# Optimization experiments

Measured on AMD Instinct MI355X. Metric: run time of the kernel, lower is better.

The kernel has to match this reference:

```python
import jax, jax.numpy as jnp
import numpy as np

N_OBJS = 100          # max detections / scatter buffer size
TOP_K = 100           # top_k_n peaks per channel
KP_THRES = 0.3        # score threshold before NMS
NMS_IOU = 0.5
RESIZE_H, RESIZE_W = 1536.0, 1536.0   # resize_shape (== heatmap HxW here)
H, W = 1536, 1536


def _peak_hms(hms):
    # 3x3 stride-1 SAME max pool; keep only local maxima (Base.apply_max_pool)
    hmax = jax.lax.reduce_window(hms, -jnp.inf, jax.lax.max, (1, 3, 3, 1), (1, 1, 1, 1), 'SAME')
    return jnp.where(hms == hmax, hms, 0.0)


def _top_k_loc(hms, k):
    # per-channel top-k peak coordinates -> [b, c, k, 2] (y, x) int32
    b, h, w, c = hms.shape
    flat = jnp.transpose(hms, (0, 3, 1, 2)).reshape(b, c, h * w)
    _, idx = jax.lax.top_k(flat, k)
    return jnp.stack([idx // w, idx % w], axis=-1).astype(jnp.int32)


def _iou_matrix(boxes):
    # boxes [N,4] = (y1,x1,y2,x2)
    y1, x1, y2, x2 = boxes[:, 0], boxes[:, 1], boxes[:, 2], boxes[:, 3]
    area = jnp.maximum(y2 - y1, 0.0) * jnp.maximum(x2 - x1, 0.0)
    iy1 = jnp.maximum(y1[:, None], y1[None, :]); ix1 = jnp.maximum(x1[:, None], x1[None, :])
    iy2 = jnp.minimum(y2[:, None], y2[None, :]); ix2 = jnp.minimum(x2[:, None], x2[None, :])
    inter = jnp.maximum(iy2 - iy1, 0.0) * jnp.maximum(ix2 - ix1, 0.0)
    union = area[:, None] + area[None, :] - inter
    return inter / jnp.maximum(union, 1e-8)


def _nms_single(boxes, scores):
    # greedy single-class NMS, fixed-size (combined_non_max_suppression equivalent,
    # clip_boxes=False, score_threshold=-inf); padded slots are zeros like TF.
    order = jnp.argsort(-scores)
    boxes, scores = boxes[order], scores[order]
    n = boxes.shape[0]
    iou = _iou_matrix(boxes)
    idxs = jnp.arange(n)

    def step(suppressed, inp):
        i, iou_row = inp
        keep_i = ~suppressed[i]
        return suppressed | (keep_i & (iou_row > NMS_IOU) & (idxs > i)), keep_i

    _, keep = jax.lax.scan(step, jnp.zeros(n, bool), (idxs, iou))
    perm = jnp.argsort(jnp.where(keep, 0, 1))  # stable: compact kept to front, score order preserved
    keep_s = keep[perm]
    out_boxes = jnp.where(keep_s[:, None], boxes[perm], 0.0)
    out_scores = jnp.where(keep_s, scores[perm], 0.0)
    return out_boxes, out_scores, jnp.zeros(n, jnp.float32)


def _forward(obj_heat_map, offset_map, size_maps, origin_shapes):
    resize_shape = jnp.array([RESIZE_H, RESIZE_W], jnp.float32)
    ratio = origin_shapes / resize_shape                      # [b,2]
    hms = _peak_hms(obj_heat_map)                             # [b,H,W,2]
    b = hms.shape[0]
    coors = _top_k_loc(hms, TOP_K)                            # [b,2,K,2]
    b_coors, b_lnmks = coors[:, :1], coors[:, 1:]             # obj / nose coords
    bidx = jnp.arange(b)[:, None, None]

    # nose landmark: scores at nose-channel peaks, masked mean of coords (int mean like TF)
    nose_scores = hms[bidx, b_lnmks[..., 0], b_lnmks[..., 1], 1]     # [b,1,K]
    nose_mask = nose_scores > 0.5
    cnt = jnp.maximum(jnp.sum(nose_mask), 1)
    lnmk_mean = jnp.sum(jnp.where(nose_mask[..., None], b_lnmks, 0), axis=(0, 1, 2)) // cnt
    b_lnmks_m = lnmk_mean.reshape(b, 1, 2)                    # requires b == 1 (as in original)
    b_nose_scores = jnp.where(nose_mask, nose_scores, -1.0).reshape(b, -1)

    # boxes from sizes at object peaks
    size_vals = size_maps[bidx, b_coors[..., 0], b_coors[..., 1]]    # [b,1,K,2]
    obj_scores = hms[bidx, b_coors[..., 0], b_coors[..., 1], 0]      # [b,1,K]
    centers = b_coors.astype(jnp.float32)
    tls = jnp.maximum(centers - size_vals / 2.0, 0.0)
    brs = jnp.minimum(centers + size_vals / 2.0, resize_shape - 1.0)
    bboxes = jnp.concatenate([tls, brs], axis=-1) * jnp.tile(ratio, (1, 2))[:, None, None, :]
    bboxes, scores = bboxes[:, 0], obj_scores[:, 0]           # [b,K,4], [b,K]

    # scatter masked candidates into -1-initialized buffer (tensor_scatter_nd_update equivalent)
    mask = scores > KP_THRES
    cand = jnp.where(mask[..., None], jnp.concatenate([bboxes, scores[..., None]], -1), -1.0)
    cand = jnp.pad(cand, ((0, 0), (0, N_OBJS - TOP_K), (0, 0)), constant_values=-1.0)  # [b,N_OBJS,5]

    nb, ns, nc = jax.vmap(_nms_single)(cand[..., :4], cand[..., 4])
    box_results = jnp.where(nb == -1.0, jnp.inf, nb)
    box_results = jnp.where(box_results == 0.0, jnp.inf, box_results)  # (x - 1 == -1)
    b_bboxes = jnp.concatenate([box_results, ns[..., None], nc[..., None]], axis=-1)  # [b,N_OBJS,6]

    # offset vectors at the mean nose landmark (gather 8ch -> [b,n,4,2])
    bidx2 = jnp.arange(b)[:, None]
    off = offset_map[bidx2, b_lnmks_m[..., 0], b_lnmks_m[..., 1]].reshape(b, 1, 4, 2)
    lf = b_lnmks_m.astype(jnp.float32)
    b_ENM = (lf[:, :, None, :] - off) * ratio[:, None, None, :]
    b_lnmks_out = lf * ratio[:, None, :]
    return b_bboxes, b_lnmks_out, b_ENM, b_nose_scores


def setup_inputs() -> dict:
    key = jax.random.key(0)
    k1, k2, k3 = jax.random.split(key, 3)
    obj_heat_map = jax.random.uniform(k1, (1, H, W, 2), jnp.float32)
    offset_map = jax.random.normal(k2, (1, H, W, 8), jnp.float32) * 8.0
    size_maps = jax.random.uniform(k3, (1, H, W, 2), jnp.float32) * 128.0
    origin_shapes = jnp.array([[1080.0, 1920.0]], jnp.float32)
    return {"obj_heat_map": obj_heat_map, "offset_map": offset_map,
            "size_maps": size_maps, "origin_shapes": origin_shapes}


def reference(obj_heat_map, offset_map, size_maps, origin_shapes):
    return _forward(obj_heat_map, offset_map, size_maps, origin_shapes)
```

## Files before the change

### kernel.cpp

```cpp
#include <hip/hip_runtime.h>
#include <cstdint>

#define IW 1536
#define IH 1536
#define TOPK 100
#define CAPP 327680
#define CAPB 128
#define CAPT 8192
#define BF_INF16 0x7F7Fu

#define NBLK 192
#define VBTOT 576

typedef unsigned u32; typedef unsigned long long u64; typedef unsigned short u16;

#define OH1   0
#define OCNT  4096
#define OSEL  4102
#define OLSD  4106
#define OBAR  4170
#define OZEND 4172
#define OPK   4172
#define OPV   (OPK + 2*CAPP)
#define OLB   (OPV + CAPP)
#define OLT   (OLB + 4*CAPB)

__device__ __forceinline__ u32 enc16(u32 b){ b &= 0xFFFFu; return (b & 0x8000u) ? ((~b)&0xFFFFu) : (b|0x8000u); }
__device__ __forceinline__ u32 dec16(u32 e){ return (e & 0x8000u) ? (e^0x8000u) : ((~e)&0xFFFFu); }
__device__ __forceinline__ float up16(u32 b){ return __uint_as_float((b&0xFFFFu)<<16); }
__device__ __forceinline__ u16 f2bf(float f){ u32 u=__float_as_uint(f); return (u16)((u + 0x7FFFu + ((u>>16)&1u))>>16); }

__device__ __forceinline__ void wave_sel2048(const u32* bins, u32 need, int* Dout, u32* Aout){
  int lane = threadIdx.x & 63;
  u32 s = 0;
  #pragma unroll
  for(int k=0;k<32;++k) s += bins[lane*32+k];
  u32 c = s;
  #pragma unroll
  for(int off=1;off<64;off<<=1){
    u32 v = __shfl_down(c, off, 64);
    if(lane + off < 64) c += v;
  }
  u32 cnext = __shfl_down(c, 1, 64); if(lane==63) cnext = 0u;
  u64 m = __ballot(c >= need);
  if(m == 0ull){ if(lane==0){ *Dout = 0; *Aout = 0u; } return; }
  int L = 63 - __builtin_clzll((unsigned long long)m);
  if(lane == L){
    u32 above = cnext; int D = 32*L;
    for(int b=32*L+31; b>=32*L; --b){
      u32 h = bins[b];
      if(above + h >= need){ D = b; break; }
      above += h;
    }
    *Dout = D; *Aout = above;
  }
}

union SMem {
  struct {
    u32 lh[4096];
    u32 lbuf[2][1600];
    u16 vbuf[2][1600];
  } a;
  struct {
    u32 lhh[4096];
    u64 tbuf[2][2048];
    u32 lsdl[64];
  } b;
  struct {
    u32 tidxS[2][CAPT];
    u32 h2s[2][2048];
    u64 keysS[2][CAPB];
    u32 selS[2][CAPB];
    u32 wbitsS[2][64];
    u32 lsdS[64];
    u32 hdr[10];
    float oval[TOPK]; int oidx[TOPK];
    float nval[TOPK]; int nidx[TOPK];
    float cbox[TOPK][4]; float cscore[TOPK]; float area[TOPK];
    int sup[TOPK]; int slotv[TOPK];
    u64 nbits[2*TOPK];
  } c;
};

__global__ __launch_bounds__(1024, 4) void fused_kernel(
    const u32* __restrict__ hm, u32* __restrict__ ws,
    const u32* __restrict__ szm, const u16* __restrict__ offm,
    const u16* __restrict__ orig, u16* __restrict__ out){
  __shared__ SMem S;
  __shared__ u32 lcnt[2], lbase[2], tcnt[2], tbase[2];
  __shared__ int Dsh[2]; __shared__ u32 Ash[2];
  __shared__ int selcS[2], selc2S[2], BvS[2], LshS[2], tcS[2];
  __shared__ u64 suppS[2];
  __shared__ int cS, srS, scS, meanr, meanc;

  int tid = threadIdx.x, lane = tid & 63;

  for(int i=tid;i<4096;i+=1024) S.a.lh[i]=0u;
  for(int vb = blockIdx.x; vb < VBTOT; vb += NBLK){
    __syncthreads();
    if(tid<2) lcnt[tid]=0u;
    __syncthreads();

    int p = (vb*1024 + tid)*4;
    int y = p / IW, x = p - y*IW;
    const u32* R1 = hm + y*IW;
    const u32* R0 = y ? R1 - IW : R1;
    const u32* R2 = (y < IH-1) ? R1 + IW : R1;
    uint4 c0 = *(const uint4*)(R0+x), c1 = *(const uint4*)(R1+x), c2 = *(const uint4*)(R2+x);
    int xl = x ? x-1 : 0, xr = (x+4 < IW) ? x+4 : IW-1;
    u32 a0[6] = {R0[xl], c0.x, c0.y, c0.z, c0.w, R0[xr]};
    u32 a1[6] = {R1[xl], c1.x, c1.y, c1.z, c1.w, R1[xr]};
    u32 a2[6] = {R2[xl], c2.x, c2.y, c2.z, c2.w, R2[xr]};

    #pragma unroll
    for(int j=0;j<4;++j){
      u32 cc = a1[j+1];
      u32 cl = cc & 0xFFFFu, chv = cc >> 16;
      u32 m0=0u, m1=0u;
      #pragma unroll
      for(int d=0;d<3;++d){
        u32 n0=a0[j+d], n2=a2[j+d]; u32 t;
        t=n0&0xFFFFu; m0=t>m0?t:m0;  t=n0>>16; m1=t>m1?t:m1;
        t=n2&0xFFFFu; m0=t>m0?t:m0;  t=n2>>16; m1=t>m1?t:m1;
      }
      { u32 n=a1[j];   u32 t=n&0xFFFFu; m0=t>m0?t:m0; t=n>>16; m1=t>m1?t:m1; }
      { u32 n=a1[j+2]; u32 t=n&0xFFFFu; m0=t>m0?t:m0; t=n>>16; m1=t>m1?t:m1; }
      bool pk0 = (cl >= m0), pk1 = (chv >= m1);
      u32 idx = (u32)(p + j);

      u64 mk0 = __ballot(pk0);
      if(mk0){
        u32 cw = __popcll(mk0), b;
        if(lane==0) b = atomicAdd(&lcnt[0], cw);
        b = __shfl(b, 0);
        if(pk0){
          u32 pos = b + __popcll(mk0 & ((1ull<<lane)-1ull));
          if(pos < 1600){ S.a.lbuf[0][pos] = idx; S.a.vbuf[0][pos] = (u16)cl; }
        }
      }
      u64 mk1 = __ballot(pk1);
      if(mk1){
        u32 cw = __popcll(mk1), b;
        if(lane==0) b = atomicAdd(&lcnt[1], cw);
        b = __shfl(b, 0);
        if(pk1){
          u32 pos = b + __popcll(mk1 & ((1ull<<lane)-1ull));
          if(pos < 1600){ S.a.lbuf[1][pos] = idx; S.a.vbuf[1][pos] = (u16)chv; }
        }
      }
      if(pk0) atomicAdd(&S.a.lh[enc16(cl)>>5], 1u);
      if(pk1) atomicAdd(&S.a.lh[2048 + (enc16(chv)>>5)], 1u);
    }
    __syncthreads();
    if(tid < 2){
      u32 n = lcnt[tid]; if(n > 1600) n = 1600;
      lcnt[tid] = n;
      lbase[tid] = atomicAdd(&ws[OCNT+tid], n);
    }
    __syncthreads();
    {
      u16* pvw = (u16*)(ws + OPV);
      for(int ch2=0;ch2<2;++ch2){
        u32 n = lcnt[ch2], base = lbase[ch2];
        for(u32 i=tid;i<n;i+=1024){
          u32 g = base + i;
          if(g < CAPP){ ws[OPK + ch2*CAPP + g] = S.a.lbuf[ch2][i]; pvw[ch2*CAPP + g] = S.a.vbuf[ch2][i]; }
        }
      }
    }
  }
  __syncthreads();
  for(int i=tid;i<4096;i+=1024) if(S.a.lh[i]) atomicAdd(&ws[OH1+i], S.a.lh[i]);

  __syncthreads();
  if(tid==0){
    __hip_atomic_fetch_add(&ws[OBAR], 1u, __ATOMIC_RELEASE, __HIP_MEMORY_SCOPE_AGENT);
    while(__hip_atomic_load(&ws[OBAR], __ATOMIC_ACQUIRE, __HIP_MEMORY_SCOPE_AGENT) < (u32)NBLK)
      __builtin_amdgcn_s_sleep(2);
  }
  __syncthreads();

  for(int i=tid;i<4096;i+=1024) S.b.lhh[i] = ws[OH1+i];
  if(tid < 2) tcnt[tid] = 0u;
  if(tid < 64) S.b.lsdl[tid] = 0u;
  __syncthreads();
  if(tid < 64)       wave_sel2048(S.b.lhh,        (u32)TOPK, &Dsh[0], &Ash[0]);
  else if(tid < 128) wave_sel2048(S.b.lhh + 2048, (u32)TOPK, &Dsh[1], &Ash[1]);
  __syncthreads();
  if(blockIdx.x == 0 && tid < 2){ ws[OSEL+tid] = (u32)Dsh[tid]; ws[OSEL+2+tid] = Ash[tid]; }

  {
    const u16* pvr = (const u16*)(ws + OPV);
    u64* listBw = (u64*)(ws + OLB);
    for(int ch2=0;ch2<2;++ch2){
      u32 n = ws[OCNT+ch2]; if(n > CAPP) n = CAPP;
      int D2 = Dsh[ch2];
      for(u32 base = blockIdx.x*1024; base < n; base += (u32)NBLK*1024){
        u32 i = base + tid;
        bool act = (i < n);
        u32 e = 0, idx = 0;
        if(act){ e = enc16(pvr[ch2*CAPP + i]); idx = ws[OPK + ch2*CAPP + i]; }
        if(act && (int)(e>>5) > D2){
          u32 pos = atomicAdd(&ws[OCNT+2+ch2], 1u);
          if(pos < CAPB) listBw[ch2*CAPB + pos] = ((u64)e<<32) | (u32)(~idx);
        }
        bool isT = act && ((int)(e>>5) == D2);
        if(isT) atomicAdd(&S.b.lsdl[ch2*32 + (e & 31u)], 1u);
        u64 mk = __ballot(isT);
        if(mk){
          u32 cw = __popcll(mk), b;
          if(lane==0) b = atomicAdd(&tcnt[ch2], cw);
          b = __shfl(b, 0);
          if(isT){
            u32 pos = b + __popcll(mk & ((1ull<<lane)-1ull));
            if(pos < 2048) S.b.tbuf[ch2][pos] = ((u64)e<<32) | (u32)(~idx);
          }
        }
      }
    }
  }
  __syncthreads();
  if(tid < 2){
    u32 c = tcnt[tid]; if(c > 2048) c = 2048;
    tcnt[tid] = c;
    tbase[tid] = atomicAdd(&ws[OCNT+4+tid], c);
  }
  __syncthreads();
  {
    u64* tieW = (u64*)(ws + OLT);
    for(int ch2=0;ch2<2;++ch2)
      for(u32 i=tid;i<tcnt[ch2];i+=1024){
        u32 g = tbase[ch2] + i;
        if(g < CAPT) tieW[ch2*CAPT + g] = S.b.tbuf[ch2][i];
      }
  }
  if(tid < 64 && S.b.lsdl[tid]) atomicAdd(&ws[OLSD + tid], S.b.lsdl[tid]);

  __syncthreads();
  if(blockIdx.x != 0){
    if(tid==0) __hip_atomic_fetch_add(&ws[OBAR+1], 1u, __ATOMIC_RELEASE, __HIP_MEMORY_SCOPE_AGENT);
    return;
  }
  if(tid==0){
    __hip_atomic_fetch_add(&ws[OBAR+1], 1u, __ATOMIC_RELEASE, __HIP_MEMORY_SCOPE_AGENT);
    while(__hip_atomic_load(&ws[OBAR+1], __ATOMIC_ACQUIRE, __HIP_MEMORY_SCOPE_AGENT) < (u32)NBLK)
      __builtin_amdgcn_s_sleep(2);
  }
  __syncthreads();

  {
    bool act5 = (tid < 512);
    int ch = (tid >> 8) & 1, ltid = tid & 255;

    if(tid < 10) S.c.hdr[tid] = ws[OCNT + tid];
    if(tid < 64) S.c.lsdS[tid] = ws[OLSD + tid];
    for(int i=tid;i<4096;i+=1024) ((u32*)S.c.h2s)[i] = 0u;
    if(tid < 128) ((u32*)S.c.wbitsS)[tid] = 0u;
    if(tid < 4){ selcS[tid&1] = 0; selc2S[tid&1] = 0; }
    if(tid < 2){ BvS[tid] = 0; LshS[tid] = 0; tcS[tid] = 0; }
    if(tid < TOPK){ S.c.oval[tid]=0.0f; S.c.oidx[tid]=0; S.c.nval[tid]=0.0f; S.c.nidx[tid]=0; }
    __syncthreads();

    int nB=0, nT=0, D=0; u32 above=0;
    const u64* listB = nullptr; const u64* tie = nullptr;
    float* dval = nullptr; int* didx = nullptr;
    if(act5){
      nB = (int)S.c.hdr[2+ch]; if(nB > CAPB) nB = CAPB;
      nT = (int)S.c.hdr[4+ch]; if(nT > CAPT) nT = CAPT;
      D  = (int)S.c.hdr[6+ch];
      above = S.c.hdr[8+ch];
      listB = ((const u64*)(ws + OLB)) + ch*CAPB;
      tie   = ((const u64*)(ws + OLT)) + ch*CAPT;
      dval = ch ? S.c.nval : S.c.oval;
      didx = ch ? S.c.nidx : S.c.oidx;
    }

    if(act5 && ltid < 64){
      u32 h = (lane < 32) ? S.c.lsdS[ch*32 + lane] : 0u;
      u32 c = h;
      #pragma unroll
      for(int off=1;off<32;off<<=1){
        u32 v = __shfl_down(c, off, 64);
        if(lane + off < 32) c += v;
      }
      u32 need2 = (u32)TOPK - above;
      u64 m = __ballot(lane >= 1 && lane < 32 && c >= need2);
      if(lane == 0){
        LshS[ch] = m ? (63 - __builtin_clzll((unsigned long long)m)) : 0;
        selcS[ch] = nB;
      }
    }
    if(act5) for(int i=ltid;i<nB;i+=256) S.c.keysS[ch][i] = listB[i];
    __syncthreads();
    u32 thr = 0; float tval = 0.0f;
    if(act5){ thr = ((u32)D<<5) | (u32)LshS[ch]; tval = up16(dec16(thr)); }

    if(act5) for(int base2=0; base2<nT; base2+=256){
      int i = base2 + ltid;
      bool act = (i < nT);
      u64 k = 0; u32 e = 0, idx = 0;
      if(act){ k = tie[i]; e = (u32)(k>>32); idx = ~(u32)(k & 0xFFFFFFFFu); }
      if(act && e > thr){
        int pos = atomicAdd(&selcS[ch], 1); if(pos < CAPB) S.c.keysS[ch][pos] = k;
      }
      bool isT = act && (e == thr);
      u64 mk = __ballot(isT);
      if(mk){
        u32 cw = __popcll(mk), b;
        if(lane==0) b = (u32)atomicAdd(&tcS[ch], (int)cw);
        b = __shfl(b, 0);
        if(isT){
          u32 pos = b + __popcll(mk & ((1ull<<lane)-1ull));
          if(pos < CAPT) S.c.tidxS[ch][pos] = idx;
        }
      }
      if(isT) atomicAdd(&S.c.h2s[ch][idx>>11], 1u);
    }
    __syncthreads();

    int nA = 0, need = 0;
    if(act5){
      nA = selcS[ch]; if(nA > CAPB) nA = CAPB; if(nA > TOPK) nA = TOPK;
      need = TOPK - nA;
      if(ltid < nA){
        u64 kreg = S.c.keysS[ch][ltid];
        int r = 0;
        for(int j=0;j<nA;++j) r += (S.c.keysS[ch][j] > kreg);
        if(r < TOPK){
          dval[r] = up16(dec16((u32)(kreg>>32)));
          didx[r] = (int)(~(u32)(kreg & 0xFFFFFFFFu));
        }
      }
      if(ltid < 64){
        const u32* hh = S.c.h2s[ch];
        int base = lane*32;
        u32 s = 0;
        #pragma unroll
        for(int k2=0;k2<32;++k2) s += hh[base+k2];
        u32 c = s;
        #pragma unroll
        for(int off=1;off<64;off<<=1){
          u32 v = __shfl_up(c, off, 64);
          if(lane >= off) c += v;
        }
        u64 m = __ballot(need > 0 && c >= (u32)need);
        int L = m ? (int)(__ffsll((unsigned long long)m) - 1) : -1;
        if(L >= 0 && lane == L){
          u32 hb[32];
          #pragma unroll
          for(int k2=0;k2<32;++k2) hb[k2] = hh[base+k2];
          u32 cum2 = c - s;
          int Bsel = base;
          #pragma unroll
          for(int k2=0;k2<32;++k2){
            if(cum2 + hb[k2] >= (u32)need){ Bsel = base+k2; break; }
            cum2 += hb[k2];
          }
          BvS[ch] = Bsel;
        }
      }
    }
    __syncthreads();

    int B = 0, tc = 0;
    if(act5){
      B = BvS[ch];
      tc = tcS[ch]; if(tc > CAPT) tc = CAPT;
      if(need > 0){
        for(int i=ltid;i<tc;i+=256){
          u32 idx = S.c.tidxS[ch][i];
          int b = (int)(idx>>11);
          if(b < B){
            int pos = atomicAdd(&selc2S[ch], 1);
            if(pos < CAPB) S.c.selS[ch][pos] = idx;
          } else if(b == B){
            atomicOr(&S.c.wbitsS[ch][(idx&2047)>>5], 1u<<(idx&31));
          }
        }
      }
    }
    __syncthreads();

    if(act5){
      int sc = selc2S[ch]; if(sc > CAPB) sc = CAPB;
      if(need > 0 && ltid < sc){
        u32 v = S.c.selS[ch][ltid];
        int r = 0;
        for(int j=0;j<sc;++j) r += (S.c.selS[ch][j] < v);
        if(nA + r < TOPK){ dval[nA+r] = tval; didx[nA+r] = (int)v; }
      }
      if(need > 0 && ltid < 64){
        u32 bits = S.c.wbitsS[ch][ltid];
        u32 cnt = __popc(bits);
        u32 incl = cnt;
        #pragma unroll
        for(int off=1;off<64;off<<=1){
          u32 v = __shfl_up(incl, off, 64);
          if(lane >= off) incl += v;
        }
        int excl = (int)(incl - cnt);
        int rem = need - sc;
        int pos = nA + sc + excl;
        int j = 0;
        while(bits){
          int l = __ffs(bits) - 1; bits &= bits - 1;
          if(excl + j < rem && pos + j < TOPK){
            dval[pos+j] = tval;
            didx[pos+j] = (int)(((u32)B<<11) | ((u32)ltid<<5) | (u32)l);
          }
          ++j;
        }
      }
    }
    __syncthreads();

    float ry = up16(orig[0]) / 1536.0f;
    float rx = up16(orig[1]) / 1536.0f;

    if(tid == 0){ cS = 0; srS = 0; scS = 0; }
    __syncthreads();
    if(tid < TOPK && S.c.nval[tid] > 0.5f){
      atomicAdd(&cS, 1);
      atomicAdd(&srS, S.c.nidx[tid] / IW);
      atomicAdd(&scS, S.c.nidx[tid] % IW);
    }
    if(tid < TOPK) out[610 + tid] = f2bf(S.c.nval[tid] > 0.5f ? S.c.nval[tid] : -1.0f);
    __syncthreads();
    if(tid == 0){
      int c = cS < 1 ? 1 : cS;
      meanr = srS / c; meanc = scS / c;
    }

    if(tid < TOPK){
      int idx = S.c.oidx[tid];
      int r = idx / IW, c = idx - r*IW;
      float score = S.c.oval[tid];
      u32 sz = szm[idx];
      float sy = up16(sz), sx = up16(sz>>16);
      float cy = (float)r, cx = (float)c;
      float tly = fmaxf(cy - sy*0.5f, 0.0f);
      float tlx = fmaxf(cx - sx*0.5f, 0.0f);
      float bry = fminf(cy + sy*0.5f, 1535.0f);
      float brx = fminf(cx + sx*0.5f, 1535.0f);
      bool mk = score > 0.3f;
      float b0 = mk ? tly*ry : -1.0f;
      float b1 = mk ? tlx*rx : -1.0f;
      float b2 = mk ? bry*ry : -1.0f;
      float b3 = mk ? brx*rx : -1.0f;
      S.c.cbox[tid][0]=b0; S.c.cbox[tid][1]=b1; S.c.cbox[tid][2]=b2; S.c.cbox[tid][3]=b3;
      S.c.cscore[tid] = mk ? score : -1.0f;
      S.c.area[tid] = fmaxf(b2-b0,0.0f) * fmaxf(b3-b1,0.0f);
    }
    if(tid < 2*TOPK) S.c.nbits[tid] = 0ull;
    __syncthreads();

    for(int t=tid; t<TOPK*TOPK; t+=1024){
      int i = t / TOPK, j = t - i*TOPK;
      if(j > i){
        float iy1 = fmaxf(S.c.cbox[i][0], S.c.cbox[j][0]);
        float ix1 = fmaxf(S.c.cbox[i][1], S.c.cbox[j][1]);
        float iy2 = fminf(S.c.cbox[i][2], S.c.cbox[j][2]);
        float ix2 = fminf(S.c.cbox[i][3], S.c.cbox[j][3]);
        float inter = fmaxf(iy2-iy1,0.0f) * fmaxf(ix2-ix1,0.0f);
        float uni = (S.c.area[i] + S.c.area[j]) - inter;
        if(inter / fmaxf(uni, 1e-8f) > 0.5f)
          atomicOr(&S.c.nbits[i*2 + (j>>6)], 1ull << (j&63));
      }
    }
    __syncthreads();
    if(tid == 0){
      u64 s0 = 0ull, s1 = 0ull;
      for(int base=0;base<TOPK;base+=10){
        u64 buf[20];
        #pragma unroll
        for(int k=0;k<20;++k) buf[k] = S.c.nbits[2*base+k];
        #pragma unroll
        for(int k=0;k<10;++k){
          int i = base+k;
          bool su = (i<64) ? ((s0>>i)&1ull) : ((s1>>(i-64))&1ull);
          if(!su){ s0 |= buf[2*k]; s1 |= buf[2*k+1]; }
        }
      }
      suppS[0] = s0; suppS[1] = s1;
    }
    __syncthreads();
    if(tid < TOPK) S.c.sup[tid] = (int)((suppS[tid>>6] >> (tid&63)) & 1ull);
    __syncthreads();

    if(tid < TOPK){
      int kbefore = 0, sbefore = 0, ktot = 0;
      for(int j=0;j<TOPK;++j){
        int sj = S.c.sup[j];
        ktot += (1 - sj);
        if(j < tid){ kbefore += (1 - sj); sbefore += sj; }
      }
      int slot = S.c.sup[tid] ? (ktot + sbefore) : kbefore;
      S.c.slotv[slot] = tid;
    }
    __syncthreads();

    if(tid < TOPK){
      int s = S.c.slotv[tid];
      bool ks = !S.c.sup[s];
      u16 row[6];
      if(ks){
        for(int d=0;d<4;++d){
          float v = S.c.cbox[s][d];
          row[d] = (v == -1.0f || v == 0.0f) ? (u16)BF_INF16 : f2bf(v);
        }
        row[4] = f2bf(S.c.cscore[s]);
      } else {
        for(int d=0;d<4;++d) row[d] = (u16)BF_INF16;
        row[4] = 0;
      }
      row[5] = 0;
      for(int d=0;d<6;++d) out[tid*6 + d] = row[d];
    }

    if(tid == 0){
      float lfy = (float)meanr, lfx = (float)meanc;
      out[600] = f2bf(lfy * ry);
      out[601] = f2bf(lfx * rx);
      const u16* op = offm + ((size_t)meanr*IW + meanc)*8;
      for(int p=0;p<4;++p){
        out[602 + p*2 + 0] = f2bf((lfy - up16(op[p*2+0])) * ry);
        out[602 + p*2 + 1] = f2bf((lfx - up16(op[p*2+1])) * rx);
      }
    }
  }
}

extern "C" void kernel_launch(void* const* d_in, const int* in_sizes, int n_in,
                              void* d_out, int out_size, void* d_ws, size_t ws_size,
                              hipStream_t stream) {
  const u32* heat = (const u32*)d_in[0];
  const u16* offm = (const u16*)d_in[1];
  const u32* szm  = (const u32*)d_in[2];
  const u16* orig = (const u16*)d_in[3];
  u16* out = (u16*)d_out;
  u32* ws = (u32*)d_ws;

  hipMemsetAsync(ws, 0, OZEND*sizeof(u32), stream);
  fused_kernel<<<NBLK, 1024, 0, stream>>>(heat, ws, szm, offm, orig, out);
}
```

Measured before the change: 197.3 us.

## Use dynamic work stealing, wider grid and per-channel final blocks

Raises the grid from 192 to 448 blocks. Heatmap chunks are now claimed through a global atomic counter, so blocks balance the peak-finding work themselves. The candidate scan becomes a single pass per block. The final top-k/NMS stage is split so block 0 handles the object channel and block 1 the nose channel, instead of one block running both. To make room, the large shared tie-index buffer moves to global workspace and the other shared buffers shrink, which should let more blocks stay resident. The grid-wide spin barriers now depend on all 448 blocks being co-resident, and the tighter launch bounds may force register spills.

```diff
diff --git a/kernel.cpp b/kernel.cpp
--- a/kernel.cpp
+++ b/kernel.cpp
@@ -9,7 +9,7 @@
 #define CAPT 8192
 #define BF_INF16 0x7F7Fu
 
-#define NBLK 192
+#define NBLK 448
 #define VBTOT 576
 
 typedef unsigned u32; typedef unsigned long long u64; typedef unsigned short u16;
@@ -19,8 +19,9 @@
 #define OSEL  4102
 #define OLSD  4106
 #define OBAR  4170
-#define OZEND 4172
-#define OPK   4172
+#define OWRK  4172
+#define OZEND 4176
+#define OPK   4176
 #define OPV   (OPK + 2*CAPP)
 #define OLB   (OPV + CAPP)
 #define OLT   (OLB + 4*CAPB)
@@ -64,43 +65,52 @@
   } a;
   struct {
     u32 lhh[4096];
-    u64 tbuf[2][2048];
+    u64 tbuf[2][1024];
     u32 lsdl[64];
   } b;
   struct {
-    u32 tidxS[2][CAPT];
-    u32 h2s[2][2048];
-    u64 keysS[2][CAPB];
-    u32 selS[2][CAPB];
-    u32 wbitsS[2][64];
-    u32 lsdS[64];
+    u32 h2s[2048];
+    u64 keysS[CAPB];
+    u32 selS[CAPB];
+    u32 wbitsS[64];
+    u32 lsdS[32];
     u32 hdr[10];
-    float oval[TOPK]; int oidx[TOPK];
-    float nval[TOPK]; int nidx[TOPK];
+    float val[TOPK]; int vidx[TOPK];
     float cbox[TOPK][4]; float cscore[TOPK]; float area[TOPK];
     int sup[TOPK]; int slotv[TOPK];
     u64 nbits[2*TOPK];
   } c;
 };
 
-__global__ __launch_bounds__(1024, 4) void fused_kernel(
+__device__ __forceinline__ void grid_arrive(u32* ctr){
+  __hip_atomic_fetch_add(ctr, 1u, __ATOMIC_RELEASE, __HIP_MEMORY_SCOPE_AGENT);
+}
+__device__ __forceinline__ void grid_wait(u32* ctr, u32 target){
+  while(__hip_atomic_load(ctr, __ATOMIC_ACQUIRE, __HIP_MEMORY_SCOPE_AGENT) < target)
+    __builtin_amdgcn_s_sleep(2);
+}
+
+__global__ __launch_bounds__(1024, 8) void fused_kernel(
     const u32* __restrict__ hm, u32* __restrict__ ws,
     const u32* __restrict__ szm, const u16* __restrict__ offm,
     const u16* __restrict__ orig, u16* __restrict__ out){
   __shared__ SMem S;
   __shared__ u32 lcnt[2], lbase[2], tcnt[2], tbase[2];
   __shared__ int Dsh[2]; __shared__ u32 Ash[2];
-  __shared__ int selcS[2], selc2S[2], BvS[2], LshS[2], tcS[2];
+  __shared__ int selcS, selc2S, BvS, LshS, tcS, vbS;
   __shared__ u64 suppS[2];
-  __shared__ int cS, srS, scS, meanr, meanc;
+  __shared__ int cS, srS, scS;
 
   int tid = threadIdx.x, lane = tid & 63;
 
   for(int i=tid;i<4096;i+=1024) S.a.lh[i]=0u;
-  for(int vb = blockIdx.x; vb < VBTOT; vb += NBLK){
-    __syncthreads();
+  for(;;){
+    __syncthreads();
+    if(tid==0) vbS = (int)atomicAdd(&ws[OWRK], 1u);
     if(tid<2) lcnt[tid]=0u;
     __syncthreads();
+    int vb = vbS;
+    if(vb >= VBTOT) break;
 
     int p = (vb*1024 + tid)*4;
     int y = p / IW, x = p - y*IW;
@@ -170,15 +180,10 @@
       }
     }
   }
-  __syncthreads();
   for(int i=tid;i<4096;i+=1024) if(S.a.lh[i]) atomicAdd(&ws[OH1+i], S.a.lh[i]);
 
   __syncthreads();
-  if(tid==0){
-    __hip_atomic_fetch_add(&ws[OBAR], 1u, __ATOMIC_RELEASE, __HIP_MEMORY_SCOPE_AGENT);
-    while(__hip_atomic_load(&ws[OBAR], __ATOMIC_ACQUIRE, __HIP_MEMORY_SCOPE_AGENT) < (u32)NBLK)
-      __builtin_amdgcn_s_sleep(2);
-  }
+  if(tid==0){ grid_arrive(&ws[OBAR]); grid_wait(&ws[OBAR], (u32)NBLK); }
   __syncthreads();
 
   for(int i=tid;i<4096;i+=1024) S.b.lhh[i] = ws[OH1+i];
@@ -196,33 +201,31 @@
     for(int ch2=0;ch2<2;++ch2){
       u32 n = ws[OCNT+ch2]; if(n > CAPP) n = CAPP;
       int D2 = Dsh[ch2];
-      for(u32 base = blockIdx.x*1024; base < n; base += (u32)NBLK*1024){
-        u32 i = base + tid;
-        bool act = (i < n);
-        u32 e = 0, idx = 0;
-        if(act){ e = enc16(pvr[ch2*CAPP + i]); idx = ws[OPK + ch2*CAPP + i]; }
-        if(act && (int)(e>>5) > D2){
-          u32 pos = atomicAdd(&ws[OCNT+2+ch2], 1u);
-          if(pos < CAPB) listBw[ch2*CAPB + pos] = ((u64)e<<32) | (u32)(~idx);
-        }
-        bool isT = act && ((int)(e>>5) == D2);
-        if(isT) atomicAdd(&S.b.lsdl[ch2*32 + (e & 31u)], 1u);
-        u64 mk = __ballot(isT);
-        if(mk){
-          u32 cw = __popcll(mk), b;
-          if(lane==0) b = atomicAdd(&tcnt[ch2], cw);
-          b = __shfl(b, 0);
-          if(isT){
-            u32 pos = b + __popcll(mk & ((1ull<<lane)-1ull));
-            if(pos < 2048) S.b.tbuf[ch2][pos] = ((u64)e<<32) | (u32)(~idx);
-          }
+      u32 i = blockIdx.x*1024 + tid;
+      bool act = (i < n);
+      u32 e = 0, idx = 0;
+      if(act){ e = enc16(pvr[ch2*CAPP + i]); idx = ws[OPK + ch2*CAPP + i]; }
+      if(act && (int)(e>>5) > D2){
+        u32 pos = atomicAdd(&ws[OCNT+2+ch2], 1u);
+        if(pos < CAPB) listBw[ch2*CAPB + pos] = ((u64)e<<32) | (u32)(~idx);
+      }
+      bool isT = act && ((int)(e>>5) == D2);
+      if(isT) atomicAdd(&S.b.lsdl[ch2*32 + (e & 31u)], 1u);
+      u64 mk = __ballot(isT);
+      if(mk){
+        u32 cw = __popcll(mk), b;
+        if(lane==0) b = atomicAdd(&tcnt[ch2], cw);
+        b = __shfl(b, 0);
+        if(isT){
+          u32 pos = b + __popcll(mk & ((1ull<<lane)-1ull));
+          if(pos < 1024) S.b.tbuf[ch2][pos] = ((u64)e<<32) | (u32)(~idx);
         }
       }
     }
   }
   __syncthreads();
   if(tid < 2){
-    u32 c = tcnt[tid]; if(c > 2048) c = 2048;
+    u32 c = tcnt[tid]; if(c > 1024) c = 1024;
     tcnt[tid] = c;
     tbase[tid] = atomicAdd(&ws[OCNT+4+tid], c);
   }
@@ -238,46 +241,32 @@
   if(tid < 64 && S.b.lsdl[tid]) atomicAdd(&ws[OLSD + tid], S.b.lsdl[tid]);
 
   __syncthreads();
-  if(blockIdx.x != 0){
-    if(tid==0) __hip_atomic_fetch_add(&ws[OBAR+1], 1u, __ATOMIC_RELEASE, __HIP_MEMORY_SCOPE_AGENT);
-    return;
-  }
-  if(tid==0){
-    __hip_atomic_fetch_add(&ws[OBAR+1], 1u, __ATOMIC_RELEASE, __HIP_MEMORY_SCOPE_AGENT);
-    while(__hip_atomic_load(&ws[OBAR+1], __ATOMIC_ACQUIRE, __HIP_MEMORY_SCOPE_AGENT) < (u32)NBLK)
-      __builtin_amdgcn_s_sleep(2);
-  }
+  if(tid==0) grid_arrive(&ws[OBAR+1]);
+  if(blockIdx.x >= 2) return;
+  if(tid==0) grid_wait(&ws[OBAR+1], (u32)NBLK);
   __syncthreads();
 
   {
-    bool act5 = (tid < 512);
-    int ch = (tid >> 8) & 1, ltid = tid & 255;
+    int ch = (int)blockIdx.x;
 
     if(tid < 10) S.c.hdr[tid] = ws[OCNT + tid];
-    if(tid < 64) S.c.lsdS[tid] = ws[OLSD + tid];
-    for(int i=tid;i<4096;i+=1024) ((u32*)S.c.h2s)[i] = 0u;
-    if(tid < 128) ((u32*)S.c.wbitsS)[tid] = 0u;
-    if(tid < 4){ selcS[tid&1] = 0; selc2S[tid&1] = 0; }
-    if(tid < 2){ BvS[tid] = 0; LshS[tid] = 0; tcS[tid] = 0; }
-    if(tid < TOPK){ S.c.oval[tid]=0.0f; S.c.oidx[tid]=0; S.c.nval[tid]=0.0f; S.c.nidx[tid]=0; }
-    __syncthreads();
-
-    int nB=0, nT=0, D=0; u32 above=0;
-    const u64* listB = nullptr; const u64* tie = nullptr;
-    float* dval = nullptr; int* didx = nullptr;
-    if(act5){
-      nB = (int)S.c.hdr[2+ch]; if(nB > CAPB) nB = CAPB;
-      nT = (int)S.c.hdr[4+ch]; if(nT > CAPT) nT = CAPT;
-      D  = (int)S.c.hdr[6+ch];
-      above = S.c.hdr[8+ch];
-      listB = ((const u64*)(ws + OLB)) + ch*CAPB;
-      tie   = ((const u64*)(ws + OLT)) + ch*CAPT;
-      dval = ch ? S.c.nval : S.c.oval;
-      didx = ch ? S.c.nidx : S.c.oidx;
-    }
-
-    if(act5 && ltid < 64){
-      u32 h = (lane < 32) ? S.c.lsdS[ch*32 + lane] : 0u;
+    if(tid < 32) S.c.lsdS[tid] = ws[OLSD + ch*32 + tid];
+    for(int i=tid;i<2048;i+=1024) S.c.h2s[i] = 0u;
+    if(tid < 64) S.c.wbitsS[tid] = 0u;
+    if(tid == 0){ selcS = 0; selc2S = 0; BvS = 0; LshS = 0; tcS = 0; }
+    if(tid < TOPK){ S.c.val[tid]=0.0f; S.c.vidx[tid]=0; }
+    __syncthreads();
+
+    int nB = (int)S.c.hdr[2+ch]; if(nB > CAPB) nB = CAPB;
+    int nT = (int)S.c.hdr[4+ch]; if(nT > CAPT) nT = CAPT;
+    int D  = (int)S.c.hdr[6+ch];
+    u32 above = S.c.hdr[8+ch];
+    const u64* listB = ((const u64*)(ws + OLB)) + ch*CAPB;
+    const u64* tie   = ((const u64*)(ws + OLT)) + ch*CAPT;
+    u32* tidxG = ws + OPK + ch*CAPT;
+
+    if(tid < 64){
+      u32 h = (lane < 32) ? S.c.lsdS[lane] : 0u;
       u32 c = h;
       #pragma unroll
       for(int off=1;off<32;off<<=1){
@@ -287,130 +276,122 @@
       u32 need2 = (u32)TOPK - above;
       u64 m = __ballot(lane >= 1 && lane < 32 && c >= need2);
       if(lane == 0){
-        LshS[ch] = m ? (63 - __builtin_clzll((unsigned long long)m)) : 0;
-        selcS[ch] = nB;
-      }
-    }
-    if(act5) for(int i=ltid;i<nB;i+=256) S.c.keysS[ch][i] = listB[i];
-    __syncthreads();
-    u32 thr = 0; float tval = 0.0f;
-    if(act5){ thr = ((u32)D<<5) | (u32)LshS[ch]; tval = up16(dec16(thr)); }
-
-    if(act5) for(int base2=0; base2<nT; base2+=256){
-      int i = base2 + ltid;
+        LshS = m ? (63 - __builtin_clzll((unsigned long long)m)) : 0;
+        selcS = nB;
+      }
+    }
+    for(int i=tid;i<nB;i+=1024) S.c.keysS[i] = listB[i];
+    __syncthreads();
+    u32 thr = ((u32)D<<5) | (u32)LshS;
+    float tval = up16(dec16(thr));
+
+    for(int base2=0; base2<nT; base2+=1024){
+      int i = base2 + tid;
       bool act = (i < nT);
       u64 k = 0; u32 e = 0, idx = 0;
       if(act){ k = tie[i]; e = (u32)(k>>32); idx = ~(u32)(k & 0xFFFFFFFFu); }
       if(act && e > thr){
-        int pos = atomicAdd(&selcS[ch], 1); if(pos < CAPB) S.c.keysS[ch][pos] = k;
+        int pos = atomicAdd(&selcS, 1); if(pos < CAPB) S.c.keysS[pos] = k;
       }
       bool isT = act && (e == thr);
       u64 mk = __ballot(isT);
       if(mk){
         u32 cw = __popcll(mk), b;
-        if(lane==0) b = (u32)atomicAdd(&tcS[ch], (int)cw);
+        if(lane==0) b = (u32)atomicAdd(&tcS, (int)cw);
         b = __shfl(b, 0);
         if(isT){
           u32 pos = b + __popcll(mk & ((1ull<<lane)-1ull));
-          if(pos < CAPT) S.c.tidxS[ch][pos] = idx;
-        }
-      }
-      if(isT) atomicAdd(&S.c.h2s[ch][idx>>11], 1u);
-    }
-    __syncthreads();
-
-    int nA = 0, need = 0;
-    if(act5){
-      nA = selcS[ch]; if(nA > CAPB) nA = CAPB; if(nA > TOPK) nA = TOPK;
-      need = TOPK - nA;
-      if(ltid < nA){
-        u64 kreg = S.c.keysS[ch][ltid];
-        int r = 0;
-        for(int j=0;j<nA;++j) r += (S.c.keysS[ch][j] > kreg);
-        if(r < TOPK){
-          dval[r] = up16(dec16((u32)(kreg>>32)));
-          didx[r] = (int)(~(u32)(kreg & 0xFFFFFFFFu));
-        }
-      }
-      if(ltid < 64){
-        const u32* hh = S.c.h2s[ch];
-        int base = lane*32;
-        u32 s = 0;
+          if(pos < CAPT) tidxG[pos] = idx;
+        }
+      }
+      if(isT) atomicAdd(&S.c.h2s[idx>>11], 1u);
+    }
+    __syncthreads();
+
+    int nA = selcS; if(nA > CAPB) nA = CAPB; if(nA > TOPK) nA = TOPK;
+    int need = TOPK - nA;
+    if(tid < nA){
+      u64 kreg = S.c.keysS[tid];
+      int r = 0;
+      for(int j=0;j<nA;++j) r += (S.c.keysS[j] > kreg);
+      if(r < TOPK){
+        S.c.val[r] = up16(dec16((u32)(kreg>>32)));
+        S.c.vidx[r] = (int)(~(u32)(kreg & 0xFFFFFFFFu));
+      }
+    }
+    if(tid < 64){
+      const u32* hh = S.c.h2s;
+      int base = lane*32;
+      u32 s = 0;
+      #pragma unroll
+      for(int k2=0;k2<32;++k2) s += hh[base+k2];
+      u32 c = s;
+      #pragma unroll
+      for(int off=1;off<64;off<<=1){
+        u32 v = __shfl_up(c, off, 64);
+        if(lane >= off) c += v;
+      }
+      u64 m = __ballot(need > 0 && c >= (u32)need);
+      int L = m ? (int)(__ffsll((unsigned long long)m) - 1) : -1;
+      if(L >= 0 && lane == L){
+        u32 hb[32];
         #pragma unroll
-        for(int k2=0;k2<32;++k2) s += hh[base+k2];
-        u32 c = s;
+        for(int k2=0;k2<32;++k2) hb[k2] = hh[base+k2];
+        u32 cum2 = c - s;
+        int Bsel = base;
         #pragma unroll
-        for(int off=1;off<64;off<<=1){
-          u32 v = __shfl_up(c, off, 64);
-          if(lane >= off) c += v;
-        }
-        u64 m = __ballot(need > 0 && c >= (u32)need);
-        int L = m ? (int)(__ffsll((unsigned long long)m) - 1) : -1;
-        if(L >= 0 && lane == L){
-          u32 hb[32];
-          #pragma unroll
-          for(int k2=0;k2<32;++k2) hb[k2] = hh[base+k2];
-          u32 cum2 = c - s;
-          int Bsel = base;
-          #pragma unroll
-          for(int k2=0;k2<32;++k2){
-            if(cum2 + hb[k2] >= (u32)need){ Bsel = base+k2; break; }
-            cum2 += hb[k2];
-          }
-          BvS[ch] = Bsel;
-        }
-      }
-    }
-    __syncthreads();
-
-    int B = 0, tc = 0;
-    if(act5){
-      B = BvS[ch];
-      tc = tcS[ch]; if(tc > CAPT) tc = CAPT;
-      if(need > 0){
-        for(int i=ltid;i<tc;i+=256){
-          u32 idx = S.c.tidxS[ch][i];
-          int b = (int)(idx>>11);
-          if(b < B){
-            int pos = atomicAdd(&selc2S[ch], 1);
-            if(pos < CAPB) S.c.selS[ch][pos] = idx;
-          } else if(b == B){
-            atomicOr(&S.c.wbitsS[ch][(idx&2047)>>5], 1u<<(idx&31));
-          }
-        }
-      }
-    }
-    __syncthreads();
-
-    if(act5){
-      int sc = selc2S[ch]; if(sc > CAPB) sc = CAPB;
-      if(need > 0 && ltid < sc){
-        u32 v = S.c.selS[ch][ltid];
-        int r = 0;
-        for(int j=0;j<sc;++j) r += (S.c.selS[ch][j] < v);
-        if(nA + r < TOPK){ dval[nA+r] = tval; didx[nA+r] = (int)v; }
-      }
-      if(need > 0 && ltid < 64){
-        u32 bits = S.c.wbitsS[ch][ltid];
-        u32 cnt = __popc(bits);
-        u32 incl = cnt;
-        #pragma unroll
-        for(int off=1;off<64;off<<=1){
-          u32 v = __shfl_up(incl, off, 64);
-          if(lane >= off) incl += v;
-        }
-        int excl = (int)(incl - cnt);
-        int rem = need - sc;
-        int pos = nA + sc + excl;
-        int j = 0;
-        while(bits){
-          int l = __ffs(bits) - 1; bits &= bits - 1;
-          if(excl + j < rem && pos + j < TOPK){
-            dval[pos+j] = tval;
-            didx[pos+j] = (int)(((u32)B<<11) | ((u32)ltid<<5) | (u32)l);
-          }
-          ++j;
-        }
+        for(int k2=0;k2<32;++k2){
+          if(cum2 + hb[k2] >= (u32)need){ Bsel = base+k2; break; }
+          cum2 += hb[k2];
+        }
+        BvS = Bsel;
+      }
+    }
+    __syncthreads();
+
+    int B = BvS;
+    int tc = tcS; if(tc > CAPT) tc = CAPT;
+    if(need > 0){
+      for(int i=tid;i<tc;i+=1024){
+        u32 idx = tidxG[i];
+        int b = (int)(idx>>11);
+        if(b < B){
+          int pos = atomicAdd(&selc2S, 1);
+          if(pos < CAPB) S.c.selS[pos] = idx;
+        } else if(b == B){
+          atomicOr(&S.c.wbitsS[(idx&2047)>>5], 1u<<(idx&31));
+        }
+      }
+    }
+    __syncthreads();
+
+    int sc = selc2S; if(sc > CAPB) sc = CAPB;
+    if(need > 0 && tid < sc){
+      u32 v = S.c.selS[tid];
+      int r = 0;
+      for(int j=0;j<sc;++j) r += (S.c.selS[j] < v);
+      if(nA + r < TOPK){ S.c.val[nA+r] = tval; S.c.vidx[nA+r] = (int)v; }
+    }
+    if(need > 0 && tid < 64){
+      u32 bits = S.c.wbitsS[tid];
+      u32 cnt = __popc(bits);
+      u32 incl = cnt;
+      #pragma unroll
+      for(int off=1;off<64;off<<=1){
+        u32 v = __shfl_up(incl, off, 64);
+        if(lane >= off) incl += v;
+      }
+      int excl = (int)(incl - cnt);
+      int rem = need - sc;
+      int pos = nA + sc + excl;
+      int j = 0;
+      while(bits){
+        int l = __ffs(bits) - 1; bits &= bits - 1;
+        if(excl + j < rem && pos + j < TOPK){
+          S.c.val[pos+j] = tval;
+          S.c.vidx[pos+j] = (int)(((u32)B<<11) | ((u32)tid<<5) | (u32)l);
+        }
+        ++j;
       }
     }
     __syncthreads();
@@ -418,24 +399,35 @@
     float ry = up16(orig[0]) / 1536.0f;
     float rx = up16(orig[1]) / 1536.0f;
 
-    if(tid == 0){ cS = 0; srS = 0; scS = 0; }
-    __syncthreads();
-    if(tid < TOPK && S.c.nval[tid] > 0.5f){
-      atomicAdd(&cS, 1);
-      atomicAdd(&srS, S.c.nidx[tid] / IW);
-      atomicAdd(&scS, S.c.nidx[tid] % IW);
-    }
-    if(tid < TOPK) out[610 + tid] = f2bf(S.c.nval[tid] > 0.5f ? S.c.nval[tid] : -1.0f);
-    __syncthreads();
-    if(tid == 0){
-      int c = cS < 1 ? 1 : cS;
-      meanr = srS / c; meanc = scS / c;
+    if(ch == 1){
+      if(tid == 0){ cS = 0; srS = 0; scS = 0; }
+      __syncthreads();
+      if(tid < TOPK && S.c.val[tid] > 0.5f){
+        atomicAdd(&cS, 1);
+        atomicAdd(&srS, S.c.vidx[tid] / IW);
+        atomicAdd(&scS, S.c.vidx[tid] % IW);
+      }
+      if(tid < TOPK) out[610 + tid] = f2bf(S.c.val[tid] > 0.5f ? S.c.val[tid] : -1.0f);
+      __syncthreads();
+      if(tid == 0){
+        int c = cS < 1 ? 1 : cS;
+        int meanr = srS / c, meanc = scS / c;
+        float lfy = (float)meanr, lfx = (float)meanc;
+        out[600] = f2bf(lfy * ry);
+        out[601] = f2bf(lfx * rx);
+        const u16* op = offm + ((size_t)meanr*IW + meanc)*8;
+        for(int p=0;p<4;++p){
+          out[602 + p*2 + 0] = f2bf((lfy - up16(op[p*2+0])) * ry);
+          out[602 + p*2 + 1] = f2bf((lfx - up16(op[p*2+1])) * rx);
+        }
+      }
+      return;
     }
 
     if(tid < TOPK){
-      int idx = S.c.oidx[tid];
+      int idx = S.c.vidx[tid];
       int r = idx / IW, c = idx - r*IW;
-      float score = S.c.oval[tid];
+      float score = S.c.val[tid];
       u32 sz = szm[idx];
       float sy = up16(sz), sx = up16(sz>>16);
       float cy = (float)r, cx = (float)c;
@@ -517,17 +509,6 @@
       row[5] = 0;
       for(int d=0;d<6;++d) out[tid*6 + d] = row[d];
     }
-
-    if(tid == 0){
-      float lfy = (float)meanr, lfx = (float)meanc;
-      out[600] = f2bf(lfy * ry);
-      out[601] = f2bf(lfx * rx);
-      const u16* op = offm + ((size_t)meanr*IW + meanc)*8;
-      for(int p=0;p<4;++p){
-        out[602 + p*2 + 0] = f2bf((lfy - up16(op[p*2+0])) * ry);
-        out[602 + p*2 + 1] = f2bf((lfx - up16(op[p*2+1])) * rx);
-      }
-    }
   }
 }
 
```

Result: slower. 223.2 us (+13.1%).
